# Optimization experiments

Hardware: AMD Instinct MI355X
Metric: run time of the kernel (lower is better)

The kernel has to match this reference:

```python
import jax, jax.numpy as jnp
import numpy as np

D_MODEL = 2048
N_HEADS = 16
N_KV = 4
HEAD_DIM = 128
SUB = 64
WINDOW = 512
THETA = 10000.0
NEG = jnp.float32(-1e30)


def _rope_tables(seq_len):
    inv_freq = 1.0 / (THETA ** (jnp.arange(0, HEAD_DIM, 2, dtype=jnp.float32) / HEAD_DIM))
    freqs = jnp.arange(seq_len, dtype=jnp.float32)[:, None] * inv_freq[None, :]  # [S, hd/2]
    emb = jnp.concatenate([freqs, freqs], axis=-1)  # [S, hd]
    return jnp.cos(emb), jnp.sin(emb)


def _rotate_half(x):
    x1, x2 = x[..., : HEAD_DIM // 2], x[..., HEAD_DIM // 2 :]
    return jnp.concatenate([-x2, x1], axis=-1)


def _apply_rope(t, cos, sin):
    # t: [B, H, S, hd]; cos/sin: [S, hd]
    c = cos[None, None]
    s = sin[None, None]
    return t * c + _rotate_half(t) * s


def setup_inputs() -> dict:
    key = jax.random.key(0)
    ks = jax.random.split(key, 6)
    B, S = 1, 2048
    std = 0.02
    return {
        "x": jax.random.normal(ks[0], (B, S, D_MODEL), dtype=jnp.float32),
        "Wq": jax.random.normal(ks[1], (D_MODEL, N_HEADS * HEAD_DIM), dtype=jnp.float32) * std,
        "Wk": jax.random.normal(ks[2], (D_MODEL, N_KV * HEAD_DIM), dtype=jnp.float32) * std,
        "Wv": jax.random.normal(ks[3], (D_MODEL, N_KV * HEAD_DIM), dtype=jnp.float32) * std,
        "Wo": jax.random.normal(ks[4], (N_HEADS * HEAD_DIM, D_MODEL), dtype=jnp.float32) * std,
        "lam": jnp.full((N_HEADS,), 0.1, dtype=jnp.float32),
    }


def reference(x, Wq, Wk, Wv, Wo, lam):
    B, S, _ = x.shape
    n_rep = N_HEADS // N_KV

    q = (x @ Wq).reshape(B, S, N_HEADS, HEAD_DIM).transpose(0, 2, 1, 3)  # [B,H,S,hd]
    k = (x @ Wk).reshape(B, S, N_KV, HEAD_DIM).transpose(0, 2, 1, 3)    # [B,KH,S,hd]
    v = (x @ Wv).reshape(B, S, N_KV, HEAD_DIM).transpose(0, 2, 1, 3)

    cos, sin = _rope_tables(S)
    q = _apply_rope(q, cos, sin)
    k = _apply_rope(k, cos, sin)

    # GQA repeat: each kv head replicated n_rep times consecutively
    k = jnp.repeat(k, n_rep, axis=1)  # [B,H,S,hd]
    v = jnp.repeat(v, n_rep, axis=1)

    q1, q2 = q[..., :SUB], q[..., SUB:]
    k1, k2 = k[..., :SUB], k[..., SUB:]
    scale = 1.0 / jnp.sqrt(jnp.float32(SUB))

    s1 = jnp.einsum("bhqd,bhkd->bhqk", q1, k1) * scale
    s2 = jnp.einsum("bhqd,bhkd->bhqk", q2, k2) * scale

    i = jnp.arange(S)[:, None]
    j = jnp.arange(S)[None, :]
    allowed = (j <= i) & (j >= i - WINDOW + 1)  # causal + sliding window
    s1 = jnp.where(allowed[None, None], s1, NEG)
    s2 = jnp.where(allowed[None, None], s2, NEG)

    a1 = jax.nn.softmax(s1.astype(jnp.float32), axis=-1).astype(x.dtype)
    a2 = jax.nn.softmax(s2.astype(jnp.float32), axis=-1).astype(x.dtype)

    diff = jax.nn.relu(a1 - lam[None, :, None, None] * a2)
    diff = diff / (jnp.sum(diff, axis=-1, keepdims=True) + 1e-6)

    out = jnp.einsum("bhqk,bhkd->bhqd", diff, v)  # [B,H,S,hd]
    out = out.transpose(0, 2, 1, 3).reshape(B, S, N_HEADS * HEAD_DIM)
    return out @ Wo
```

## Files before the change

kernel.cpp:

```cpp
#include <hip/hip_runtime.h>
#include <hip/hip_bf16.h>
#include <stdint.h>

typedef __attribute__((ext_vector_type(8))) short short8;
typedef __attribute__((ext_vector_type(4))) float f32x4;
using bf16 = __hip_bfloat16;

#define MFMA16(a, b, c) __builtin_amdgcn_mfma_f32_16x16x32_bf16((a), (b), (c), 0, 0, 0)

#define GLOAD_LDS16(g, l) __builtin_amdgcn_global_load_lds( \
    (const __attribute__((address_space(1))) void*)(g),     \
    (__attribute__((address_space(3))) void*)(l), 16, 0, 0)

__device__ __forceinline__ unsigned packbf2(float lo, float hi) {
  unsigned r;
  asm("v_cvt_pk_bf16_f32 %0, %1, %2" : "=v"(r) : "v"(lo), "v"(hi));
  return r;
}
__device__ __forceinline__ float ex2(float x) {
  float r;
  asm("v_exp_f32 %0, %1" : "=v"(r) : "v"(x));
  return r;
}
__device__ __forceinline__ f32x4 vmax4(f32x4 a, f32x4 b) {
  f32x4 r;
  r[0] = fmaxf(a[0], b[0]); r[1] = fmaxf(a[1], b[1]);
  r[2] = fmaxf(a[2], b[2]); r[3] = fmaxf(a[3], b[3]);
  return r;
}

template <bool EDGE>
__device__ __forceinline__ void p1_update(const f32x4* sv, float& m, float& l,
                                          int kb0, int myq, int lhi) {
  f32x4 t4 = vmax4(vmax4(sv[0], sv[1]), vmax4(sv[2], sv[3]));
  float tm = fmaxf(fmaxf(t4[0], t4[1]), fmaxf(t4[2], t4[3]));
  float nm = fmaxf(m, tm);
  float sc = ex2(m - nm);
  float sum = 0.f;
#pragma unroll
  for (int nt = 0; nt < 4; ++nt) {
    float part = 0.f;
#pragma unroll
    for (int r = 0; r < 4; ++r) {
      float e = ex2(sv[nt][r] - nm);
      if (EDGE) {
        int key = kb0 + nt * 16 + lhi * 4 + r;
        bool ok = (key <= myq) && (key > myq - 512);
        e = ok ? e : 0.f;
      }
      part += e;
    }
    sum += part;
  }
  l = l * sc + sum;
  m = nm;
}

template <bool EDGE>
__device__ __forceinline__ float p2_probs(const f32x4* s1v, const f32x4* s2v,
                                          float m1, float m2, float c2,
                                          int kb0, int myq, int lhi, int l15,
                                          unsigned* pw) {
  float d0 = 0.f, d1 = 0.f;
#pragma unroll
  for (int nt = 0; nt < 4; ++nt) {
    float pr[4];
#pragma unroll
    for (int r = 0; r < 4; ++r) {
      float e1 = ex2(s1v[nt][r] - m1);
      float e2 = ex2(s2v[nt][r] - m2);
      float p = fmaf(-c2, e2, e1);
      p = fmaxf(p, 0.f);
      if (EDGE) {
        int key = kb0 + nt * 16 + lhi * 4 + r;
        bool ok = (key <= myq) && (key > myq - 512);
        p = ok ? p : 0.f;
      }
      pr[r] = p;
      if (r & 1) d1 += p; else d0 += p;
    }
    int pi = l15 * 36 + 8 * nt + 2 * lhi;
    pw[pi]     = packbf2(pr[0], pr[1]);
    pw[pi + 1] = packbf2(pr[2], pr[3]);
  }
  return d0 + d1;
}

__global__ __launch_bounds__(256) void prep_all(const float* __restrict__ x,
                                                const float* __restrict__ Wq,
                                                const float* __restrict__ Wk,
                                                const float* __restrict__ Wv,
                                                const float* __restrict__ Wo,
                                                bf16* __restrict__ xb,
                                                bf16* __restrict__ WqkvFT,
                                                bf16* __restrict__ WoFT)
{
  const int bx = blockIdx.x;
  const int tid = threadIdx.x;
  if (bx >= 80) {
    size_t i = ((size_t)(bx - 80) * 32 + blockIdx.y) * 2048 + tid * 8;
    const float* f = x + i;
    float4 a = *(const float4*)f;
    float4 b = *(const float4*)(f + 4);
    union { bf16 h[8]; short8 s; } u;
    u.h[0] = __float2bfloat16(a.x); u.h[1] = __float2bfloat16(a.y);
    u.h[2] = __float2bfloat16(a.z); u.h[3] = __float2bfloat16(a.w);
    u.h[4] = __float2bfloat16(b.x); u.h[5] = __float2bfloat16(b.y);
    u.h[6] = __float2bfloat16(b.z); u.h[7] = __float2bfloat16(b.w);
    *(short8*)(xb + i) = u.s;
    return;
  }
  const float* W;
  bf16* Wt;
  int N, n0;
  if (bx < 32)      { W = Wq; Wt = WqkvFT; N = 2048; n0 = bx * 64; }
  else if (bx < 40) { W = Wk; Wt = WqkvFT; N = 512;  n0 = 2048 + (bx - 32) * 64; }
  else if (bx < 48) { W = Wv; Wt = WqkvFT; N = 512;  n0 = 2560 + (bx - 40) * 64; }
  else              { W = Wo; Wt = WoFT;   N = 2048; n0 = (bx - 48) * 64; }
  const int nloc0 = (N == 512) ? (n0 - ((n0 >= 2560) ? 2560 : 2048)) : ((bx < 32 || bx >= 48) ? (n0 & 2047) : 0);
  const int k0 = blockIdx.y * 64;

  __shared__ bf16 t[64][72];
#pragma unroll
  for (int pass = 0; pass < 4; ++pass) {
    int r = pass * 16 + (tid >> 4);
    int c = (tid & 15) * 4;
    float4 v = *(const float4*)(W + (size_t)(k0 + r) * N + nloc0 + c);
    t[c + 0][r] = __float2bfloat16(v.x);
    t[c + 1][r] = __float2bfloat16(v.y);
    t[c + 2][r] = __float2bfloat16(v.z);
    t[c + 3][r] = __float2bfloat16(v.w);
  }
  __syncthreads();
#pragma unroll
  for (int pass = 0; pass < 2; ++pass) {
    int n = pass * 32 + (tid >> 3);
    int k8 = (tid & 7) * 8;
    int frag = ((n0 + n) >> 4) * 64 + ((k0 + k8) >> 5);
    int ln = (n & 15) + 16 * ((k8 >> 3) & 3);
    *(short8*)(Wt + (size_t)frag * 512 + ln * 8) = *(const short8*)(&t[n][k8]);
  }
}

template <int EPI>
__global__ __launch_bounds__(256) void gemm_ft(const bf16* __restrict__ A,
                                               const bf16* __restrict__ Bft,
                                               void* __restrict__ C,
                                               bf16* __restrict__ VTp,
                                               int M, int N, int K)
{
  __shared__ __align__(16) bf16 As[4][128 * 32];

  const int tid  = threadIdx.x;
  const int lane = tid & 63;
  const int w    = tid >> 6;
  const int wmg  = (w >> 1) * 4;
  const int wng  = (w & 1) * 4;
  const int l15  = lane & 15;
  const int lhi  = lane >> 4;
  const int bm0  = blockIdx.y * 128;
  const int bn0  = blockIdx.x * 128;

  const int srow = lane >> 2;
  const int scol = ((lane & 3) ^ ((lane >> 3) & 3)) * 8;
  const int loff = l15 * 4 + (lhi ^ ((l15 >> 1) & 3));

  const int nkc = K >> 5;
  const bf16* bbase[4];
#pragma unroll
  for (int nt = 0; nt < 4; ++nt)
    bbase[nt] = Bft + ((size_t)((bn0 >> 4) + wng + nt) * nkc) * 512 + lane * 8;

  f32x4 acc[4][4];
  const f32x4 zero4 = {0.f, 0.f, 0.f, 0.f};
#pragma unroll
  for (int i = 0; i < 4; ++i)
#pragma unroll
    for (int j = 0; j < 4; ++j) acc[i][j] = zero4;

  short8 br0[4], br1[4], br2[4], br3[4];

#define GSTAGE_A(buf, kk)                                                          \
  { _Pragma("unroll")                                                              \
    for (int p = 0; p < 2; ++p) {                                                  \
      int s   = (p * 4 + w) * 64 + lane;                                           \
      int row = (p * 4 + w) * 16 + srow;                                           \
      GLOAD_LDS16(A + (size_t)(bm0 + row) * K + (kk) + scol, &As[buf][s * 8]);     \
    } }

#define BLOAD(breg, kc)                                                            \
  { _Pragma("unroll")                                                              \
    for (int nt = 0; nt < 4; ++nt) {                                               \
      asm volatile("global_load_dwordx4 %0, %1, off"                               \
                   : "=v"(breg[nt])                                                \
                   : "v"(bbase[nt] + (size_t)(kc) * 512)                           \
                   : "memory");                                                    \
    } }

#define KSTEP(aslot, breg, wcn, ...)                                               \
  {                                                                                \
    asm volatile("s_waitcnt vmcnt(" #wcn ")" ::: "memory");                        \
    __builtin_amdgcn_s_barrier();                                                  \
    __builtin_amdgcn_sched_barrier(0);                                             \
    __VA_ARGS__                                                                    \
    short8 a_[4];                                                                  \
    _Pragma("unroll")                                                              \
    for (int mt = 0; mt < 4; ++mt)                                                 \
      a_[mt] = *(const short8*)(&As[aslot][((wmg + mt) * 64 + loff) * 8]);         \
    _Pragma("unroll")                                                              \
    for (int mt = 0; mt < 4; ++mt)                                                 \
      _Pragma("unroll")                                                            \
      for (int nt = 0; nt < 4; ++nt)                                               \
        acc[mt][nt] = MFMA16(a_[mt], breg[nt], acc[mt][nt]);                       \
  }

  GSTAGE_A(0, 0);  BLOAD(br0, 0);
  GSTAGE_A(1, 32); BLOAD(br1, 1);
  GSTAGE_A(2, 64); BLOAD(br2, 2);

  for (int t = 0; t < nkc - 4; t += 4) {
    KSTEP(0, br0, 12, GSTAGE_A(3, (t + 3) * 32); BLOAD(br3, t + 3);)
    KSTEP(1, br1, 12, GSTAGE_A(0, (t + 4) * 32); BLOAD(br0, t + 4);)
    KSTEP(2, br2, 12, GSTAGE_A(1, (t + 5) * 32); BLOAD(br1, t + 5);)
    KSTEP(3, br3, 12, GSTAGE_A(2, (t + 6) * 32); BLOAD(br2, t + 6);)
  }
  KSTEP(0, br0, 12, GSTAGE_A(3, (nkc - 1) * 32); BLOAD(br3, nkc - 1);)
  KSTEP(1, br1, 12, )
  KSTEP(2, br2, 6, )
  KSTEP(3, br3, 0, )
#undef GSTAGE_A
#undef BLOAD
#undef KSTEP

  if (EPI == 1) {
#pragma unroll
    for (int mt = 0; mt < 4; ++mt) {
      int row0 = bm0 + (wmg + mt) * 16 + lhi * 4;
#pragma unroll
      for (int nt = 0; nt < 4; ++nt) {
        int col = bn0 + (wng + nt) * 16 + l15;
#pragma unroll
        for (int r = 0; r < 4; ++r)
          ((float*)C)[(size_t)(row0 + r) * N + col] = acc[mt][nt][r];
      }
    }
    return;
  }

  __syncthreads();
  if (bn0 < 2560) {
    float* Lf = (float*)&As[0][0];
    const float scale = (bn0 < 2048) ? 0.180336880111120f : 1.0f;
#pragma unroll
    for (int c = 0; c < 2; ++c) {
      if ((w >> 1) == c) {
#pragma unroll
        for (int mt = 0; mt < 4; ++mt)
#pragma unroll
          for (int nt = 0; nt < 4; ++nt) {
            int col = (wng + nt) * 16 + l15;
#pragma unroll
            for (int r = 0; r < 4; ++r)
              Lf[(mt * 16 + lhi * 4 + r) * 128 + col] = acc[mt][nt][r];
          }
      }
      __syncthreads();
      {
        int rloc = tid >> 2;
        int dg = (tid & 3) * 16;
        int s = bm0 + c * 64 + rloc;
        bf16* orow = (bf16*)C + (size_t)s * N + bn0;
        union { bf16 h[16]; short8 v[2]; } o1, o2;
#pragma unroll
        for (int e = 0; e < 16; ++e) {
          int d = dg + e;
          float inv = __expf(-(float)d * (9.210340371976184f / 64.0f));
          float ang = (float)s * inv;
          float cs = __cosf(ang), sn = __sinf(ang);
          float x1 = Lf[rloc * 128 + d];
          float x2 = Lf[rloc * 128 + d + 64];
          o1.h[e] = __float2bfloat16((x1 * cs - x2 * sn) * scale);
          o2.h[e] = __float2bfloat16((x2 * cs + x1 * sn) * scale);
        }
        *(short8*)(orow + dg)      = o1.v[0];
        *(short8*)(orow + dg + 8)  = o1.v[1];
        *(short8*)(orow + dg + 64) = o2.v[0];
        *(short8*)(orow + dg + 72) = o2.v[1];
      }
      __syncthreads();
    }
  } else {
    bf16* Lb = &As[0][0];
#pragma unroll
    for (int cc = 0; cc < 2; ++cc) {
      if ((w & 1) == cc) {
#pragma unroll
        for (int mt = 0; mt < 4; ++mt)
#pragma unroll
          for (int nt = 0; nt < 4; ++nt) {
            int colloc = nt * 16 + l15;
#pragma unroll
            for (int r = 0; r < 4; ++r) {
              int key = (wmg + mt) * 16 + lhi * 4 + r;
              Lb[colloc * 136 + key] = __float2bfloat16(acc[mt][nt][r]);
            }
          }
      }
      __syncthreads();
      {
        int dl = tid >> 2;
        int kq = (tid & 3) * 32;
        int dim = (bn0 - 2560) + cc * 64 + dl;
        bf16* vrow = VTp + (size_t)dim * 2048 + bm0 + kq;
#pragma unroll
        for (int j = 0; j < 4; ++j)
          *(short8*)(vrow + j * 8) = *(const short8*)(&Lb[dl * 136 + kq + j * 8]);
      }
      __syncthreads();
    }
  }
}

__global__ __launch_bounds__(256) void diff_attn(const bf16* __restrict__ QKV,
                                                 const bf16* __restrict__ VT,
                                                 const float* __restrict__ lam,
                                                 bf16* __restrict__ O)
{
  __shared__ __align__(16) bf16 Kb[2][64 * 128];
  __shared__ __align__(16) bf16 Vb[2][128 * 64];
  __shared__ __align__(16) bf16 Pw[4][16 * 72];

  const int qb   = blockIdx.x;
  const int h    = blockIdx.y;
  const int kvh  = h >> 2;
  const int tid  = threadIdx.x;
  const int lane = tid & 63;
  const int w    = tid >> 6;
  const int l15  = lane & 15;
  const int lhi  = lane >> 4;
  const int qg   = qb * 64 + w * 16;
  const int myq  = qg + l15;
  const float lamv = lam[h];

  const bf16* Kg = QKV + 2048 + (size_t)kvh * 128;
  const bf16* Vg = VT + (size_t)kvh * 128 * 2048;

  short8 qf[4];
  {
    const bf16* qrow = QKV + (size_t)myq * 3072 + h * 128;
#pragma unroll
    for (int c = 0; c < 4; ++c)
      qf[c] = *(const short8*)(qrow + c * 32 + lhi * 8);
  }

  const int t0 = (qb >= 8) ? (qb - 8) : 0;

#define STAGE_K(buf, kbase)                                                     \
  {                                                                             \
    _Pragma("unroll")                                                           \
    for (int p = 0; p < 4; ++p) {                                               \
      int c = p * 256 + tid;                                                    \
      int r = c >> 4, q = c & 15;                                               \
      GLOAD_LDS16(Kg + (size_t)((kbase) + r) * 3072 + ((q ^ (r & 7)) * 8),      \
                  &Kb[buf][c * 8]);                                             \
    }                                                                           \
  }
#define STAGE_V(buf, kbase)                                                     \
  {                                                                             \
    _Pragma("unroll")                                                           \
    for (int p = 0; p < 4; ++p) {                                               \
      int c = p * 256 + tid;                                                    \
      int d = c >> 3, q = c & 7;                                                \
      GLOAD_LDS16(Vg + (size_t)d * 2048 + (kbase) + ((q ^ (d & 7)) * 8),        \
                  &Vb[buf][c * 8]);                                             \
    }                                                                           \
  }
#define KFRAG(buf, nt, qc) \
  (*(const short8*)(&Kb[buf][(((nt) * 16 + l15) * 16 + ((qc) ^ (((nt) * 16 + l15) & 7))) * 8]))
#define VFRAG(buf, n, qc) \
  (*(const short8*)(&Vb[buf][(((n) * 16 + l15) * 8 + ((qc) ^ (((n) * 16 + l15) & 7))) * 8]))
#define QK_TILE(cur)                                            \
  _Pragma("unroll")                                             \
  for (int nt = 0; nt < 4; ++nt) {                              \
    f32x4 s1 = zero4, s2 = zero4;                               \
    s1 = MFMA16(KFRAG(cur, nt, lhi),      qf[0], s1);           \
    s1 = MFMA16(KFRAG(cur, nt, 4 + lhi),  qf[1], s1);           \
    s2 = MFMA16(KFRAG(cur, nt, 8 + lhi),  qf[2], s2);           \
    s2 = MFMA16(KFRAG(cur, nt, 12 + lhi), qf[3], s2);           \
    s1v[nt] = s1; s2v[nt] = s2;                                 \
  }

  const f32x4 zero4 = {0.f, 0.f, 0.f, 0.f};

  float m1 = -1e30f, l1 = 0.f, m2 = -1e30f, l2 = 0.f;
  STAGE_K(0, t0 * 64);
  __syncthreads();
  {
    int cur = 0;
    for (int t = t0; t <= qb; ++t, cur ^= 1) {
      if (t < qb) STAGE_K(cur ^ 1, (t + 1) * 64);
      const int kb0 = t * 64;
      f32x4 s1v[4], s2v[4];
      QK_TILE(cur);
      const bool edge = (t == qb) || (qb >= 8 && t == t0);
      if (edge) {
        p1_update<true>(s1v, m1, l1, kb0, myq, lhi);
        p1_update<true>(s2v, m2, l2, kb0, myq, lhi);
      } else {
        p1_update<false>(s1v, m1, l1, kb0, myq, lhi);
        p1_update<false>(s2v, m2, l2, kb0, myq, lhi);
      }
      __syncthreads();
    }
  }

#pragma unroll
  for (int mk = 16; mk <= 32; mk <<= 1) {
    float pm = __shfl_xor(m1, mk, 64), pl = __shfl_xor(l1, mk, 64);
    float M = fmaxf(m1, pm);
    l1 = l1 * ex2(m1 - M) + pl * ex2(pm - M);
    m1 = M;
    pm = __shfl_xor(m2, mk, 64); pl = __shfl_xor(l2, mk, 64);
    M = fmaxf(m2, pm);
    l2 = l2 * ex2(m2 - M) + pl * ex2(pm - M);
    m2 = M;
  }
  const float c2 = lamv * l1 / l2;

  f32x4 accv[8];
#pragma unroll
  for (int n = 0; n < 8; ++n) accv[n] = zero4;
  float dln = 0.f;

  STAGE_K(0, t0 * 64);
  STAGE_V(0, t0 * 64);
  __syncthreads();
  {
    int cur = 0;
    for (int t = t0; t <= qb; ++t, cur ^= 1) {
      if (t < qb) {
        STAGE_K(cur ^ 1, (t + 1) * 64);
        STAGE_V(cur ^ 1, (t + 1) * 64);
      }
      const int kb0 = t * 64;
      unsigned* pw = (unsigned*)&Pw[w][0];
      f32x4 s1v[4], s2v[4];
      QK_TILE(cur);
      const bool edge = (t == qb) || (qb >= 8 && t == t0);
      if (edge) dln += p2_probs<true>(s1v, s2v, m1, m2, c2, kb0, myq, lhi, l15, pw);
      else      dln += p2_probs<false>(s1v, s2v, m1, m2, c2, kb0, myq, lhi, l15, pw);
#pragma unroll
      for (int kc = 0; kc < 2; ++kc) {
        short8 pa = *(const short8*)(&Pw[w][l15 * 72 + kc * 32 + lhi * 8]);
#pragma unroll
        for (int n = 0; n < 8; ++n)
          accv[n] = MFMA16(pa, VFRAG(cur, n, kc * 4 + lhi), accv[n]);
      }
      __syncthreads();
    }
  }

  dln += __shfl_xor(dln, 16, 64);
  dln += __shfl_xor(dln, 32, 64);

#pragma unroll
  for (int r = 0; r < 4; ++r) {
    int srcq = lhi * 4 + r;
    int src = (lane & 48) | srcq;
    float dq = __shfl(dln, src, 64);
    float lq = __shfl(l1, src, 64);
    float rinv = 1.f / (dq + lq * 1e-6f);
    int qo = qg + srcq;
#pragma unroll
    for (int n = 0; n < 8; ++n) {
      O[(size_t)qo * 2048 + h * 128 + n * 16 + l15] =
          __float2bfloat16(accv[n][r] * rinv);
    }
  }
#undef STAGE_K
#undef STAGE_V
#undef KFRAG
#undef VFRAG
#undef QK_TILE
}

extern "C" void kernel_launch(void* const* d_in, const int* in_sizes, int n_in,
                              void* d_out, int out_size, void* d_ws, size_t ws_size,
                              hipStream_t stream)
{
  const float* x   = (const float*)d_in[0];
  const float* Wq  = (const float*)d_in[1];
  const float* Wk  = (const float*)d_in[2];
  const float* Wv  = (const float*)d_in[3];
  const float* Wo  = (const float*)d_in[4];
  const float* lam = (const float*)d_in[5];

  char* ws = (char*)d_ws;
  bf16* xb     = (bf16*)(ws);
  bf16* WqkvFT = (bf16*)(ws + 8ull  * (1u << 20));
  bf16* WoFT   = (bf16*)(ws + 20ull * (1u << 20));
  bf16* QKV    = (bf16*)(ws + 28ull * (1u << 20));
  bf16* ATT    = (bf16*)(ws + 40ull * (1u << 20));
  bf16* VT     = (bf16*)(ws + 48ull * (1u << 20));

  prep_all<<<dim3(144, 32), 256, 0, stream>>>(x, Wq, Wk, Wv, Wo, xb, WqkvFT, WoFT);
  gemm_ft<0><<<dim3(24, 16), 256, 0, stream>>>(xb, WqkvFT, QKV, VT, 2048, 3072, 2048);
  diff_attn<<<dim3(32, 16), 256, 0, stream>>>(QKV, VT, lam, ATT);
  gemm_ft<1><<<dim3(16, 16), 256, 0, stream>>>(ATT, WoFT, d_out, nullptr, 2048, 2048, 2048);
}
```

Baseline: 111.5 us.

## Overlap K/V prefetch with compute via partial vmcnt waits and swizzle block order

The attention loops now use raw s_barrier with partial s_waitcnt vmcnt counts, so the direct-to-LDS prefetch of the next K/V tile can stay in flight while the current tile is computed. Before, __syncthreads forced every outstanding load to drain each iteration. Both the GEMM and the attention kernel also remap block indices with an XCD-aware swizzle (stride 8), so neighbouring tiles and heads run on the same chiplet and share L2. The risks are that the hand-picked vmcnt counts must exactly match the number of loads each STAGE issues, and that the missing LDS waits could cause races.

```diff
diff --git a/kernel.cpp b/kernel.cpp
--- a/kernel.cpp
+++ b/kernel.cpp
@@ -158,8 +158,13 @@
   const int wng  = (w & 1) * 4;
   const int l15  = lane & 15;
   const int lhi  = lane >> 4;
-  const int bm0  = blockIdx.y * 128;
-  const int bn0  = blockIdx.x * 128;
+
+  const int nbx = gridDim.x;
+  const int lb  = blockIdx.y * nbx + blockIdx.x;
+  const int nwg = nbx * gridDim.y;
+  const int lsw = (lb & 7) * (nwg >> 3) + (lb >> 3);
+  const int bm0 = (lsw / nbx) * 128;
+  const int bn0 = (lsw % nbx) * 128;
 
   const int srow = lane >> 2;
   const int scol = ((lane & 3) ^ ((lane >> 3) & 3)) * 8;
@@ -330,8 +335,11 @@
   __shared__ __align__(16) bf16 Vb[2][128 * 64];
   __shared__ __align__(16) bf16 Pw[4][16 * 72];
 
-  const int qb   = blockIdx.x;
-  const int h    = blockIdx.y;
+  const int lb  = blockIdx.y * 32 + blockIdx.x;
+  const int lsw = (lb & 7) * 64 + (lb >> 3);
+  const int qb  = lsw & 31;
+  const int h   = lsw >> 5;
+
   const int kvh  = h >> 2;
   const int tid  = threadIdx.x;
   const int lane = tid & 63;
@@ -394,11 +402,19 @@
 
   float m1 = -1e30f, l1 = 0.f, m2 = -1e30f, l2 = 0.f;
   STAGE_K(0, t0 * 64);
-  __syncthreads();
+  asm volatile("s_waitcnt vmcnt(0)" ::: "memory");
+  __builtin_amdgcn_s_barrier();
   {
     int cur = 0;
     for (int t = t0; t <= qb; ++t, cur ^= 1) {
-      if (t < qb) STAGE_K(cur ^ 1, (t + 1) * 64);
+      if (t < qb) {
+        STAGE_K(cur ^ 1, (t + 1) * 64);
+        asm volatile("s_waitcnt vmcnt(4)" ::: "memory");
+      } else {
+        asm volatile("s_waitcnt vmcnt(0)" ::: "memory");
+      }
+      __builtin_amdgcn_s_barrier();
+      __builtin_amdgcn_sched_barrier(0);
       const int kb0 = t * 64;
       f32x4 s1v[4], s2v[4];
       QK_TILE(cur);
@@ -410,7 +426,7 @@
         p1_update<false>(s1v, m1, l1, kb0, myq, lhi);
         p1_update<false>(s2v, m2, l2, kb0, myq, lhi);
       }
-      __syncthreads();
+      __builtin_amdgcn_s_barrier();
     }
   }
 
@@ -434,14 +450,20 @@
 
   STAGE_K(0, t0 * 64);
   STAGE_V(0, t0 * 64);
-  __syncthreads();
+  asm volatile("s_waitcnt vmcnt(0)" ::: "memory");
+  __builtin_amdgcn_s_barrier();
   {
     int cur = 0;
     for (int t = t0; t <= qb; ++t, cur ^= 1) {
       if (t < qb) {
         STAGE_K(cur ^ 1, (t + 1) * 64);
         STAGE_V(cur ^ 1, (t + 1) * 64);
-      }
+        asm volatile("s_waitcnt vmcnt(8)" ::: "memory");
+      } else {
+        asm volatile("s_waitcnt vmcnt(0)" ::: "memory");
+      }
+      __builtin_amdgcn_s_barrier();
+      __builtin_amdgcn_sched_barrier(0);
       const int kb0 = t * 64;
       unsigned* pw = (unsigned*)&Pw[w][0];
       f32x4 s1v[4], s2v[4];
@@ -456,7 +478,7 @@
         for (int n = 0; n < 8; ++n)
           accv[n] = MFMA16(pa, VFRAG(cur, n, kc * 4 + lhi), accv[n]);
       }
-      __syncthreads();
+      __builtin_amdgcn_s_barrier();
     }
   }
 
```

Result: no change. 110.9 us (-0.6%).
